# Optimization experiments

Measured on AMD Instinct MI355X. Metric: run time of the kernel, lower is better.

Reference implementation:

```python
import jax, jax.numpy as jnp
import numpy as np

H_G, W_G = 9, 25
N_NODES = H_G * W_G  # 225


def _grid_edge_index():
    # 8-connected grid graph INCLUDING self loops (di=dj=0), matching build_grid_edge_index.
    # PyG GATConv's remove_self_loops+add_self_loops leaves this edge set unchanged.
    edges = []
    for i in range(H_G):
        for j in range(W_G):
            nid = i * W_G + j
            for di in (-1, 0, 1):
                for dj in (-1, 0, 1):
                    ni, nj = i + di, j + dj
                    if 0 <= ni < H_G and 0 <= nj < W_G:
                        edges.append((nid, ni * W_G + nj))
    return jnp.asarray(np.array(edges, dtype=np.int32).T)  # [2, 1825]


def _gat(x, edge_index, W, a_src, a_dst, bias, concat):
    # x: [B, N, F_in]; W: [F_in, heads*d]; a_src/a_dst: [heads, d]
    B = x.shape[0]
    heads, d = a_src.shape
    h = (x @ W).reshape(B, N_NODES, heads, d)          # [B,N,H,D]
    src, dst = edge_index[0], edge_index[1]            # message flows src -> dst
    asrc = jnp.einsum('bnhd,hd->bnh', h, a_src)        # [B,N,H]
    adst = jnp.einsum('bnhd,hd->bnh', h, a_dst)
    e = jax.nn.leaky_relu(asrc[:, src] + adst[:, dst], 0.2)  # [B,E,H]
    et = jnp.transpose(e, (1, 0, 2))                   # [E,B,H] (segment ops over leading axis)
    m = jax.ops.segment_max(et, dst, num_segments=N_NODES)  # [N,B,H]
    ex = jnp.exp(et - m[dst])
    s = jax.ops.segment_sum(ex, dst, num_segments=N_NODES)
    alpha = ex / s[dst]                                # softmax over incoming edges per node
    ht = jnp.transpose(h, (1, 0, 2, 3))                # [N,B,H,D]
    out = jax.ops.segment_sum(alpha[..., None] * ht[src], dst, num_segments=N_NODES)  # [N,B,H,D]
    out = jnp.transpose(out, (1, 0, 2, 3))             # [B,N,H,D]
    if concat:
        out = out.reshape(B, N_NODES, heads * d)
    else:
        out = out.mean(axis=2)
    return out + bias


def setup_inputs() -> dict:
    key = jax.random.key(0)
    ks = jax.random.split(key, 16)
    B = 128
    s = 0.02
    inp = {
        'x4': jax.random.normal(ks[0], (B, 2048, 9, 25), dtype=jnp.float32),
        'pool_w': jax.random.normal(ks[1], (8, 2048), dtype=jnp.float32) * s,
        'pool_b': jnp.zeros((8,), dtype=jnp.float32),
        'gat1_w': jax.random.normal(ks[2], (8, 64), dtype=jnp.float32) * s,
        'gat1_asrc': jax.random.normal(ks[3], (4, 16), dtype=jnp.float32) * s,
        'gat1_adst': jax.random.normal(ks[4], (4, 16), dtype=jnp.float32) * s,
        'gat1_b': jnp.zeros((64,), dtype=jnp.float32),
        'gat2_w': jax.random.normal(ks[5], (64, 8), dtype=jnp.float32) * s,
        'gat2_asrc': jax.random.normal(ks[6], (1, 8), dtype=jnp.float32) * s,
        'gat2_adst': jax.random.normal(ks[7], (1, 8), dtype=jnp.float32) * s,
        'gat2_b': jnp.zeros((8,), dtype=jnp.float32),
        'w1': jax.random.normal(ks[8], (1800, 2048), dtype=jnp.float32) * 0.01,
        'b1': jnp.zeros((2048,), dtype=jnp.float32),
        'w2': jax.random.normal(ks[9], (2048, 20800), dtype=jnp.float32) * 0.01,
        'b2': jnp.zeros((20800,), dtype=jnp.float32),
        'edge_index': _grid_edge_index(),
    }
    return inp


def reference(x4, pool_w, pool_b, gat1_w, gat1_asrc, gat1_adst, gat1_b,
              gat2_w, gat2_asrc, gat2_adst, gat2_b, w1, b1, w2, b2, edge_index):
    B = x4.shape[0]
    # 1x1 conv pool: 2048 -> 8 channels (already 9x25, adaptive_avg_pool2d is identity)
    fea = jnp.einsum('bchw,oc->bohw', x4, pool_w) + pool_b[None, :, None, None]
    fea = fea.reshape(B, 8, N_NODES).transpose(0, 2, 1)  # [B, 225, 8]
    x1 = jax.nn.relu(_gat(fea, edge_index, gat1_w, gat1_asrc, gat1_adst, gat1_b, concat=True))
    x2 = _gat(x1, edge_index, gat2_w, gat2_asrc, gat2_adst, gat2_b, concat=False)  # [B,225,8]
    flat = x2.reshape(B, -1)                             # [B, 1800]
    hid = jax.nn.relu(flat @ w1 + b1)
    out = hid @ w2 + b2
    return out.reshape(-1, 100, 52, 4)
```

## Files before the change

kernel.cpp:

```cpp
#include <hip/hip_runtime.h>
#include <hip/hip_bf16.h>


typedef __attribute__((ext_vector_type(8))) short bh8_t;
typedef __attribute__((ext_vector_type(4))) float f32x4;

static __device__ __forceinline__ short f2bs(float f) {
    __hip_bfloat16 h = __float2bfloat16(f);
    return *reinterpret_cast<short*>(&h);
}
static __device__ __forceinline__ unsigned pack2(short a, short b) {
    return (unsigned)(unsigned short)a | ((unsigned)(unsigned short)b << 16);
}

__global__ __launch_bounds__(256) void pool_kernel(const float* __restrict__ x4,
                                                   const float* __restrict__ pool_w,
                                                   float* __restrict__ part) {
    const int b  = blockIdx.x >> 3;
    const int ch = blockIdx.x & 7;
    __shared__ __align__(16) float ws[256 * 8];
    const int tid = threadIdx.x;
    for (int i = tid; i < 2048; i += 256)
        ws[i] = pool_w[(i & 7) * 2048 + ch * 256 + (i >> 3)];
    __syncthreads();
    if (tid < 225) {
        const float* xp = x4 + ((size_t)b * 2048 + (size_t)ch * 256) * 225 + tid;
        float a0 = 0, a1 = 0, a2 = 0, a3 = 0, a4 = 0, a5 = 0, a6 = 0, a7 = 0;
#pragma unroll 8
        for (int c = 0; c < 256; ++c) {
            float v = xp[c * 225];
            const float4 wa = *reinterpret_cast<const float4*>(&ws[c * 8]);
            const float4 wb = *reinterpret_cast<const float4*>(&ws[c * 8 + 4]);
            a0 += v * wa.x; a1 += v * wa.y; a2 += v * wa.z; a3 += v * wa.w;
            a4 += v * wb.x; a5 += v * wb.y; a6 += v * wb.z; a7 += v * wb.w;
        }
        float* dst = part + (size_t)b * 14400 + ch * 1800 + tid * 8;
        dst[0] = a0; dst[1] = a1; dst[2] = a2; dst[3] = a3;
        dst[4] = a4; dst[5] = a5; dst[6] = a6; dst[7] = a7;
    }
}

__global__ __launch_bounds__(256) void gat1_kernel(const float* __restrict__ part,
                                                   const float* __restrict__ pool_b,
                                                   const float* __restrict__ w,
                                                   const float* __restrict__ a_src,
                                                   const float* __restrict__ a_dst,
                                                   const float* __restrict__ bias,
                                                   float* __restrict__ x1) {
    __shared__ __align__(16) float fea[1800];
    __shared__ __align__(16) float h[14400];
    const int b = blockIdx.x;
    const int tid = threadIdx.x;

    for (int i = tid; i < 1800; i += 256) {
        const float* p = part + (size_t)b * 14400 + i;
        float s = 0;
#pragma unroll
        for (int c = 0; c < 8; ++c) s += p[c * 1800];
        fea[i] = s + pool_b[i & 7];
    }
    __syncthreads();

    {
        const int o = tid & 63, mr = tid >> 6;
        float wv[8];
#pragma unroll
        for (int k = 0; k < 8; ++k) wv[k] = w[k * 64 + o];
        for (int n = mr; n < 225; n += 4) {
            float acc = 0;
#pragma unroll
            for (int k = 0; k < 8; ++k) acc += fea[n * 8 + k] * wv[k];
            h[n * 64 + o] = acc;
        }
    }
    __syncthreads();

    for (int t = tid; t < 900; t += 256) {
        const int n = t >> 2, hd = t & 3;
        const float* hp = &h[n * 64 + hd * 16];
        float as = 0, ad = 0;
#pragma unroll
        for (int d = 0; d < 16; ++d) {
            float hv = hp[d];
            as += hv * a_src[hd * 16 + d];
            ad += hv * a_dst[hd * 16 + d];
        }
        fea[t] = as;
        fea[900 + t] = ad;
    }
    __syncthreads();

    for (int task = tid; task < 900; task += 256) {
        const int n = task >> 2, hd = task & 3;
        const int i = n / 25, j = n % 25;
        const float adn = fea[900 + task];
        float e[9];
        int sid[9];
        float mx = -1e30f;
#pragma unroll
        for (int t9 = 0; t9 < 9; ++t9) {
            const int di = t9 / 3 - 1, dj = t9 % 3 - 1;
            const int ni = i + di, nj = j + dj;
            const bool valid = ((unsigned)ni < 9u) && ((unsigned)nj < 25u);
            const int s = valid ? ni * 25 + nj : n;
            sid[t9] = s;
            float ev = fea[s * 4 + hd] + adn;
            ev = ev >= 0.f ? ev : 0.2f * ev;
            e[t9] = valid ? ev : -1e30f;
            mx = fmaxf(mx, e[t9]);
        }
        float sum = 0;
#pragma unroll
        for (int t9 = 0; t9 < 9; ++t9) {
            float ex = __expf(e[t9] - mx);
            e[t9] = ex;
            sum += ex;
        }
        const float inv = 1.f / sum;
        float out[16] = {};
#pragma unroll
        for (int t9 = 0; t9 < 9; ++t9) {
            const float al = e[t9] * inv;
            const float* hp = &h[sid[t9] * 64 + hd * 16];
#pragma unroll
            for (int d = 0; d < 16; ++d) out[d] += al * hp[d];
        }
        float* dst = x1 + (size_t)b * 14400 + n * 64 + hd * 16;
        const float* bp = bias + hd * 16;
#pragma unroll
        for (int d = 0; d < 16; ++d) dst[d] = fmaxf(out[d] + bp[d], 0.f);
    }
}

__global__ __launch_bounds__(256) void gat2_kernel(const float* __restrict__ x1,
                                                   const float* __restrict__ w,
                                                   const float* __restrict__ a_src,
                                                   const float* __restrict__ a_dst,
                                                   const float* __restrict__ bias,
                                                   short* __restrict__ flat) {
    __shared__ __align__(16) float xs[14400];
    __shared__ __align__(16) float h[1800];
    const int b = blockIdx.x;
    const int tid = threadIdx.x;
    for (int i = tid; i < 14400; i += 256) xs[i] = x1[(size_t)b * 14400 + i];
    __syncthreads();
    for (int t = tid; t < 1800; t += 256) {
        const int o = t & 7, n = t >> 3;
        float acc = 0;
#pragma unroll 8
        for (int k = 0; k < 64; ++k) acc += xs[n * 64 + k] * w[k * 8 + o];
        h[t] = acc;
    }
    __syncthreads();
    if (tid < 225) {
        const int n = tid, i = n / 25, j = n % 25;
        float av[8], dv[8];
#pragma unroll
        for (int d = 0; d < 8; ++d) { av[d] = a_src[d]; dv[d] = a_dst[d]; }
        float adn = 0;
#pragma unroll
        for (int d = 0; d < 8; ++d) adn += h[n * 8 + d] * dv[d];
        float e[9];
        int sid[9];
        float mx = -1e30f;
#pragma unroll
        for (int t9 = 0; t9 < 9; ++t9) {
            const int di = t9 / 3 - 1, dj = t9 % 3 - 1;
            const int ni = i + di, nj = j + dj;
            const bool valid = ((unsigned)ni < 9u) && ((unsigned)nj < 25u);
            const int s = valid ? ni * 25 + nj : n;
            sid[t9] = s;
            float as = 0;
#pragma unroll
            for (int d = 0; d < 8; ++d) as += h[s * 8 + d] * av[d];
            float ev = as + adn;
            ev = ev >= 0.f ? ev : 0.2f * ev;
            e[t9] = valid ? ev : -1e30f;
            mx = fmaxf(mx, e[t9]);
        }
        float sum = 0;
#pragma unroll
        for (int t9 = 0; t9 < 9; ++t9) {
            float ex = __expf(e[t9] - mx);
            e[t9] = ex;
            sum += ex;
        }
        const float inv = 1.f / sum;
        float out[8] = {};
#pragma unroll
        for (int t9 = 0; t9 < 9; ++t9) {
            const float al = e[t9] * inv;
            const float* hp = &h[sid[t9] * 8];
#pragma unroll
            for (int d = 0; d < 8; ++d) out[d] += al * hp[d];
        }
        short* dst = flat + (size_t)b * 1800 + n * 8;
#pragma unroll
        for (int d = 0; d < 8; ++d) dst[d] = f2bs(out[d] + bias[d]);
    }
}

template <int BN, int MT, int NT, int NWN, bool RELU, bool OUT_BF16>
__global__ __launch_bounds__(256) void gemm_mfma(const short* __restrict__ A,
                                                 const float* __restrict__ Wf,
                                                 const float* __restrict__ bias,
                                                 void* __restrict__ outp,
                                                 int K, int N) {
    constexpr int LDT = 40;
    __shared__ __align__(16) short sA[128 * LDT];
    __shared__ __align__(16) short sB[BN * LDT];
    const int tid = threadIdx.x;
    const int lane = tid & 63;
    const int wave = tid >> 6;
    const int n0 = blockIdx.x * BN;
    const int wm0 = (wave / NWN) * (MT * 16);
    const int wn0 = (wave % NWN) * (NT * 16);
    const int lm = lane & 15;
    const int lkb = (lane >> 4) * 8;

    const int am = tid >> 1;
    const int akh = tid & 1;
    constexpr int EPT = (32 * BN) / 256;
    const int bn_ = tid % BN;
    const int bk0 = (tid / BN) * EPT;

    f32x4 acc[MT][NT] = {};

    const int nkt = (K + 31) >> 5;
    for (int kt = 0; kt < nkt; ++kt) {
        const int k0 = kt << 5;
        if (k0 + 32 <= K) {
            const uint4* src = reinterpret_cast<const uint4*>(A + (size_t)am * K + k0 + akh * 16);
            uint4 v0 = src[0];
            uint4 v1 = src[1];
            float bv[EPT];
#pragma unroll
            for (int jj = 0; jj < EPT; ++jj)
                bv[jj] = Wf[(size_t)(k0 + bk0 + jj) * N + n0 + bn_];
            uint4* dstA = reinterpret_cast<uint4*>(&sA[am * LDT + akh * 16]);
            dstA[0] = v0;
            dstA[1] = v1;
            unsigned uw[EPT / 2];
#pragma unroll
            for (int jj = 0; jj < EPT / 2; ++jj)
                uw[jj] = pack2(f2bs(bv[2 * jj]), f2bs(bv[2 * jj + 1]));
            if constexpr (EPT == 8) {
                uint4 u;
                u.x = uw[0]; u.y = uw[1]; u.z = uw[2]; u.w = uw[3];
                *reinterpret_cast<uint4*>(&sB[bn_ * LDT + bk0]) = u;
            } else {
                *reinterpret_cast<unsigned*>(&sB[bn_ * LDT + bk0]) = uw[0];
            }
        } else {
#pragma unroll
            for (int jj = 0; jj < 16; ++jj) {
                const int kk = k0 + akh * 16 + jj;
                sA[am * LDT + akh * 16 + jj] = (kk < K) ? A[(size_t)am * K + kk] : (short)0;
            }
#pragma unroll
            for (int jj = 0; jj < EPT; ++jj) {
                const int kk = k0 + bk0 + jj;
                const float v = (kk < K) ? Wf[(size_t)kk * N + n0 + bn_] : 0.f;
                sB[bn_ * LDT + bk0 + jj] = f2bs(v);
            }
        }
        __syncthreads();
        bh8_t bfr[NT];
#pragma unroll
        for (int nt = 0; nt < NT; ++nt)
            bfr[nt] = *reinterpret_cast<const bh8_t*>(&sB[(wn0 + nt * 16 + lm) * LDT + lkb]);
#pragma unroll
        for (int mt = 0; mt < MT; ++mt) {
            bh8_t afr = *reinterpret_cast<const bh8_t*>(&sA[(wm0 + mt * 16 + lm) * LDT + lkb]);
#pragma unroll
            for (int nt = 0; nt < NT; ++nt)
                acc[mt][nt] = __builtin_amdgcn_mfma_f32_16x16x32_bf16(afr, bfr[nt], acc[mt][nt], 0, 0, 0);
        }
        __syncthreads();
    }
    const int rg = lane >> 4;
#pragma unroll
    for (int nt = 0; nt < NT; ++nt) {
        const int n = n0 + wn0 + nt * 16 + lm;
        const float bv = bias[n];
#pragma unroll
        for (int mt = 0; mt < MT; ++mt) {
#pragma unroll
            for (int r = 0; r < 4; ++r) {
                const int m = wm0 + mt * 16 + rg * 4 + r;
                float v = acc[mt][nt][r] + bv;
                if (RELU) v = fmaxf(v, 0.f);
                if (OUT_BF16)
                    reinterpret_cast<short*>(outp)[(size_t)m * N + n] = f2bs(v);
                else
                    reinterpret_cast<float*>(outp)[(size_t)m * N + n] = v;
            }
        }
    }
}

extern "C" void kernel_launch(void* const* d_in, const int* in_sizes, int n_in,
                              void* d_out, int out_size, void* d_ws, size_t ws_size,
                              hipStream_t stream) {
    const float* x4        = (const float*)d_in[0];
    const float* pool_w    = (const float*)d_in[1];
    const float* pool_b    = (const float*)d_in[2];
    const float* gat1_w    = (const float*)d_in[3];
    const float* gat1_asrc = (const float*)d_in[4];
    const float* gat1_adst = (const float*)d_in[5];
    const float* gat1_b    = (const float*)d_in[6];
    const float* gat2_w    = (const float*)d_in[7];
    const float* gat2_asrc = (const float*)d_in[8];
    const float* gat2_adst = (const float*)d_in[9];
    const float* gat2_b    = (const float*)d_in[10];
    const float* w1        = (const float*)d_in[11];
    const float* b1        = (const float*)d_in[12];
    const float* w2        = (const float*)d_in[13];
    const float* b2        = (const float*)d_in[14];
    float* out = (float*)d_out;

    char* ws = (char*)d_ws;
    float* part = (float*)ws;
    float* x1   = (float*)(ws + 7372800);
    short* flat = (short*)(ws + 14745600);
    short* hid  = (short*)(ws + 15206400);

    pool_kernel<<<1024, 256, 0, stream>>>(x4, pool_w, part);
    gat1_kernel<<<128, 256, 0, stream>>>(part, pool_b, gat1_w, gat1_asrc, gat1_adst, gat1_b, x1);
    gat2_kernel<<<128, 256, 0, stream>>>(x1, gat2_w, gat2_asrc, gat2_adst, gat2_b, flat);
    gemm_mfma<16, 2, 1, 1, true, true><<<128, 256, 0, stream>>>(flat, w1, b1, (void*)hid, 1800, 2048);
    gemm_mfma<64, 4, 2, 2, false, false><<<325, 256, 0, stream>>>(hid, w2, b2, (void*)out, 2048, 20800);
}
```

Measured before the change: 568.6 us.

## Prefetch GEMM tiles into registers, swizzle GAT LDS, vectorize stores, retile w2 GEMM

```diff
diff --git a/kernel.cpp b/kernel.cpp
--- a/kernel.cpp
+++ b/kernel.cpp
@@ -11,6 +11,12 @@
 }
 static __device__ __forceinline__ unsigned pack2(short a, short b) {
     return (unsigned)(unsigned short)a | ((unsigned)(unsigned short)b << 16);
+}
+static __device__ __forceinline__ int swz64(int n, int o) {
+    return n * 64 + ((((o >> 2) ^ (n & 15)) << 2) | (o & 3));
+}
+static __device__ __forceinline__ int swzg(int n, int g) {
+    return n * 64 + ((g ^ (n & 15)) << 2);
 }
 
 __global__ __launch_bounds__(256) void pool_kernel(const float* __restrict__ x4,
@@ -18,26 +24,29 @@
                                                    float* __restrict__ part) {
     const int b  = blockIdx.x >> 3;
     const int ch = blockIdx.x & 7;
-    __shared__ __align__(16) float ws[256 * 8];
     const int tid = threadIdx.x;
-    for (int i = tid; i < 2048; i += 256)
-        ws[i] = pool_w[(i & 7) * 2048 + ch * 256 + (i >> 3)];
-    __syncthreads();
-    if (tid < 225) {
-        const float* xp = x4 + ((size_t)b * 2048 + (size_t)ch * 256) * 225 + tid;
-        float a0 = 0, a1 = 0, a2 = 0, a3 = 0, a4 = 0, a5 = 0, a6 = 0, a7 = 0;
+    if (tid >= 225) return;
+    const float* xp = x4 + ((size_t)b * 2048 + (size_t)ch * 256) * 225 + tid;
+    const float* w0 = pool_w + 0 * 2048 + ch * 256;
+    const float* w1 = pool_w + 1 * 2048 + ch * 256;
+    const float* w2 = pool_w + 2 * 2048 + ch * 256;
+    const float* w3 = pool_w + 3 * 2048 + ch * 256;
+    const float* w4 = pool_w + 4 * 2048 + ch * 256;
+    const float* w5 = pool_w + 5 * 2048 + ch * 256;
+    const float* w6 = pool_w + 6 * 2048 + ch * 256;
+    const float* w7 = pool_w + 7 * 2048 + ch * 256;
+    float a0 = 0, a1 = 0, a2 = 0, a3 = 0, a4 = 0, a5 = 0, a6 = 0, a7 = 0;
 #pragma unroll 8
-        for (int c = 0; c < 256; ++c) {
-            float v = xp[c * 225];
-            const float4 wa = *reinterpret_cast<const float4*>(&ws[c * 8]);
-            const float4 wb = *reinterpret_cast<const float4*>(&ws[c * 8 + 4]);
-            a0 += v * wa.x; a1 += v * wa.y; a2 += v * wa.z; a3 += v * wa.w;
-            a4 += v * wb.x; a5 += v * wb.y; a6 += v * wb.z; a7 += v * wb.w;
-        }
-        float* dst = part + (size_t)b * 14400 + ch * 1800 + tid * 8;
-        dst[0] = a0; dst[1] = a1; dst[2] = a2; dst[3] = a3;
-        dst[4] = a4; dst[5] = a5; dst[6] = a6; dst[7] = a7;
-    }
+    for (int c = 0; c < 256; ++c) {
+        const float v = xp[c * 225];
+        a0 += v * w0[c]; a1 += v * w1[c]; a2 += v * w2[c]; a3 += v * w3[c];
+        a4 += v * w4[c]; a5 += v * w5[c]; a6 += v * w6[c]; a7 += v * w7[c];
+    }
+    float* dst = part + (size_t)b * 14400 + ch * 1800 + tid * 8;
+    float4 r0; r0.x = a0; r0.y = a1; r0.z = a2; r0.w = a3;
+    float4 r1; r1.x = a4; r1.y = a5; r1.z = a6; r1.w = a7;
+    *reinterpret_cast<float4*>(dst) = r0;
+    *reinterpret_cast<float4*>(dst + 4) = r1;
 }
 
 __global__ __launch_bounds__(256) void gat1_kernel(const float* __restrict__ part,
@@ -70,65 +79,90 @@
             float acc = 0;
 #pragma unroll
             for (int k = 0; k < 8; ++k) acc += fea[n * 8 + k] * wv[k];
-            h[n * 64 + o] = acc;
-        }
-    }
-    __syncthreads();
-
-    for (int t = tid; t < 900; t += 256) {
-        const int n = t >> 2, hd = t & 3;
-        const float* hp = &h[n * 64 + hd * 16];
-        float as = 0, ad = 0;
-#pragma unroll
-        for (int d = 0; d < 16; ++d) {
-            float hv = hp[d];
-            as += hv * a_src[hd * 16 + d];
-            ad += hv * a_dst[hd * 16 + d];
-        }
-        fea[t] = as;
-        fea[900 + t] = ad;
-    }
-    __syncthreads();
-
-    for (int task = tid; task < 900; task += 256) {
-        const int n = task >> 2, hd = task & 3;
-        const int i = n / 25, j = n % 25;
-        const float adn = fea[900 + task];
-        float e[9];
-        int sid[9];
-        float mx = -1e30f;
-#pragma unroll
-        for (int t9 = 0; t9 < 9; ++t9) {
-            const int di = t9 / 3 - 1, dj = t9 % 3 - 1;
-            const int ni = i + di, nj = j + dj;
-            const bool valid = ((unsigned)ni < 9u) && ((unsigned)nj < 25u);
-            const int s = valid ? ni * 25 + nj : n;
-            sid[t9] = s;
-            float ev = fea[s * 4 + hd] + adn;
-            ev = ev >= 0.f ? ev : 0.2f * ev;
-            e[t9] = valid ? ev : -1e30f;
-            mx = fmaxf(mx, e[t9]);
-        }
-        float sum = 0;
-#pragma unroll
-        for (int t9 = 0; t9 < 9; ++t9) {
-            float ex = __expf(e[t9] - mx);
-            e[t9] = ex;
-            sum += ex;
-        }
-        const float inv = 1.f / sum;
-        float out[16] = {};
-#pragma unroll
-        for (int t9 = 0; t9 < 9; ++t9) {
-            const float al = e[t9] * inv;
-            const float* hp = &h[sid[t9] * 64 + hd * 16];
-#pragma unroll
-            for (int d = 0; d < 16; ++d) out[d] += al * hp[d];
-        }
-        float* dst = x1 + (size_t)b * 14400 + n * 64 + hd * 16;
-        const float* bp = bias + hd * 16;
-#pragma unroll
-        for (int d = 0; d < 16; ++d) dst[d] = fmaxf(out[d] + bp[d], 0.f);
+            h[swz64(n, o)] = acc;
+        }
+    }
+    __syncthreads();
+
+    {
+        const int hd = tid & 3;
+        float4 asw[4], adw[4];
+#pragma unroll
+        for (int j = 0; j < 4; ++j) {
+            asw[j] = *reinterpret_cast<const float4*>(a_src + hd * 16 + 4 * j);
+            adw[j] = *reinterpret_cast<const float4*>(a_dst + hd * 16 + 4 * j);
+        }
+        for (int t = tid; t < 900; t += 256) {
+            const int n = t >> 2;
+            float as = 0, ad = 0;
+#pragma unroll
+            for (int j = 0; j < 4; ++j) {
+                const float4 hv = *reinterpret_cast<const float4*>(&h[swzg(n, 4 * hd + j)]);
+                as += hv.x * asw[j].x + hv.y * asw[j].y + hv.z * asw[j].z + hv.w * asw[j].w;
+                ad += hv.x * adw[j].x + hv.y * adw[j].y + hv.z * adw[j].z + hv.w * adw[j].w;
+            }
+            fea[t] = as;
+            fea[900 + t] = ad;
+        }
+    }
+    __syncthreads();
+
+    {
+        const int hd = tid & 3;
+        float4 b4[4];
+#pragma unroll
+        for (int j = 0; j < 4; ++j)
+            b4[j] = *reinterpret_cast<const float4*>(bias + hd * 16 + 4 * j);
+        for (int task = tid; task < 900; task += 256) {
+            const int n = task >> 2;
+            const int i = n / 25, j25 = n % 25;
+            const float adn = fea[900 + task];
+            float e[9];
+            int sid[9];
+            float mx = -1e30f;
+#pragma unroll
+            for (int t9 = 0; t9 < 9; ++t9) {
+                const int di = t9 / 3 - 1, dj = t9 % 3 - 1;
+                const int ni = i + di, nj = j25 + dj;
+                const bool valid = ((unsigned)ni < 9u) && ((unsigned)nj < 25u);
+                const int s = valid ? ni * 25 + nj : n;
+                sid[t9] = s;
+                float ev = fea[s * 4 + hd] + adn;
+                ev = ev >= 0.f ? ev : 0.2f * ev;
+                e[t9] = valid ? ev : -1e30f;
+                mx = fmaxf(mx, e[t9]);
+            }
+            float sum = 0;
+#pragma unroll
+            for (int t9 = 0; t9 < 9; ++t9) {
+                float ex = __expf(e[t9] - mx);
+                e[t9] = ex;
+                sum += ex;
+            }
+            const float inv = 1.f / sum;
+            float4 o4[4] = {};
+#pragma unroll
+            for (int t9 = 0; t9 < 9; ++t9) {
+                const float al = e[t9] * inv;
+                const int s = sid[t9];
+#pragma unroll
+                for (int jj = 0; jj < 4; ++jj) {
+                    const float4 hv = *reinterpret_cast<const float4*>(&h[swzg(s, 4 * hd + jj)]);
+                    o4[jj].x += al * hv.x; o4[jj].y += al * hv.y;
+                    o4[jj].z += al * hv.z; o4[jj].w += al * hv.w;
+                }
+            }
+            float* dst = x1 + (size_t)b * 14400 + n * 64 + hd * 16;
+#pragma unroll
+            for (int jj = 0; jj < 4; ++jj) {
+                float4 r;
+                r.x = fmaxf(o4[jj].x + b4[jj].x, 0.f);
+                r.y = fmaxf(o4[jj].y + b4[jj].y, 0.f);
+                r.z = fmaxf(o4[jj].z + b4[jj].z, 0.f);
+                r.w = fmaxf(o4[jj].w + b4[jj].w, 0.f);
+                *reinterpret_cast<float4*>(dst + 4 * jj) = r;
+            }
+        }
     }
 }
 
@@ -139,17 +173,26 @@
                                                    const float* __restrict__ bias,
                                                    short* __restrict__ flat) {
     __shared__ __align__(16) float xs[14400];
-    __shared__ __align__(16) float h[1800];
+    __shared__ __align__(16) float h2[8 * 232];
     const int b = blockIdx.x;
     const int tid = threadIdx.x;
-    for (int i = tid; i < 14400; i += 256) xs[i] = x1[(size_t)b * 14400 + i];
+    for (int i4 = tid; i4 < 3600; i4 += 256) {
+        const int n = i4 >> 4, g0 = i4 & 15;
+        const float4 v = *reinterpret_cast<const float4*>(&x1[(size_t)b * 14400 + (i4 << 2)]);
+        *reinterpret_cast<float4*>(&xs[swzg(n, g0)]) = v;
+    }
     __syncthreads();
     for (int t = tid; t < 1800; t += 256) {
         const int o = t & 7, n = t >> 3;
         float acc = 0;
-#pragma unroll 8
-        for (int k = 0; k < 64; ++k) acc += xs[n * 64 + k] * w[k * 8 + o];
-        h[t] = acc;
+#pragma unroll
+        for (int jj = 0; jj < 16; ++jj) {
+            const float4 xv = *reinterpret_cast<const float4*>(&xs[swzg(n, jj)]);
+            const int k = 4 * jj;
+            acc += xv.x * w[k * 8 + o] + xv.y * w[(k + 1) * 8 + o]
+                 + xv.z * w[(k + 2) * 8 + o] + xv.w * w[(k + 3) * 8 + o];
+        }
+        h2[o * 232 + n] = acc;
     }
     __syncthreads();
     if (tid < 225) {
@@ -159,7 +202,7 @@
         for (int d = 0; d < 8; ++d) { av[d] = a_src[d]; dv[d] = a_dst[d]; }
         float adn = 0;
 #pragma unroll
-        for (int d = 0; d < 8; ++d) adn += h[n * 8 + d] * dv[d];
+        for (int d = 0; d < 8; ++d) adn += h2[d * 232 + n] * dv[d];
         float e[9];
         int sid[9];
         float mx = -1e30f;
@@ -172,7 +215,7 @@
             sid[t9] = s;
             float as = 0;
 #pragma unroll
-            for (int d = 0; d < 8; ++d) as += h[s * 8 + d] * av[d];
+            for (int d = 0; d < 8; ++d) as += h2[d * 232 + s] * av[d];
             float ev = as + adn;
             ev = ev >= 0.f ? ev : 0.2f * ev;
             e[t9] = valid ? ev : -1e30f;
@@ -190,13 +233,15 @@
 #pragma unroll
         for (int t9 = 0; t9 < 9; ++t9) {
             const float al = e[t9] * inv;
-            const float* hp = &h[sid[t9] * 8];
-#pragma unroll
-            for (int d = 0; d < 8; ++d) out[d] += al * hp[d];
-        }
-        short* dst = flat + (size_t)b * 1800 + n * 8;
-#pragma unroll
-        for (int d = 0; d < 8; ++d) dst[d] = f2bs(out[d] + bias[d]);
+#pragma unroll
+            for (int d = 0; d < 8; ++d) out[d] += al * h2[d * 232 + sid[t9]];
+        }
+        unsigned u[4];
+#pragma unroll
+        for (int p = 0; p < 4; ++p)
+            u[p] = pack2(f2bs(out[2 * p] + bias[2 * p]), f2bs(out[2 * p + 1] + bias[2 * p + 1]));
+        uint4 uv; uv.x = u[0]; uv.y = u[1]; uv.z = u[2]; uv.w = u[3];
+        *reinterpret_cast<uint4*>(flat + (size_t)b * 1800 + n * 8) = uv;
     }
 }
 
@@ -207,6 +252,7 @@
                                                  void* __restrict__ outp,
                                                  int K, int N) {
     constexpr int LDT = 40;
+    constexpr int EPT = (32 * BN) / 256;
     __shared__ __align__(16) short sA[128 * LDT];
     __shared__ __align__(16) short sB[BN * LDT];
     const int tid = threadIdx.x;
@@ -220,51 +266,62 @@
 
     const int am = tid >> 1;
     const int akh = tid & 1;
-    constexpr int EPT = (32 * BN) / 256;
     const int bn_ = tid % BN;
     const int bk0 = (tid / BN) * EPT;
 
-    f32x4 acc[MT][NT] = {};
-
+    union { uint4 v[2]; short s[16]; } pa;
+    float pb[EPT];
     const int nkt = (K + 31) >> 5;
-    for (int kt = 0; kt < nkt; ++kt) {
+
+    auto loadg = [&](int kt) {
         const int k0 = kt << 5;
         if (k0 + 32 <= K) {
             const uint4* src = reinterpret_cast<const uint4*>(A + (size_t)am * K + k0 + akh * 16);
-            uint4 v0 = src[0];
-            uint4 v1 = src[1];
-            float bv[EPT];
+            pa.v[0] = src[0];
+            pa.v[1] = src[1];
 #pragma unroll
             for (int jj = 0; jj < EPT; ++jj)
-                bv[jj] = Wf[(size_t)(k0 + bk0 + jj) * N + n0 + bn_];
-            uint4* dstA = reinterpret_cast<uint4*>(&sA[am * LDT + akh * 16]);
-            dstA[0] = v0;
-            dstA[1] = v1;
-            unsigned uw[EPT / 2];
-#pragma unroll
-            for (int jj = 0; jj < EPT / 2; ++jj)
-                uw[jj] = pack2(f2bs(bv[2 * jj]), f2bs(bv[2 * jj + 1]));
-            if constexpr (EPT == 8) {
-                uint4 u;
-                u.x = uw[0]; u.y = uw[1]; u.z = uw[2]; u.w = uw[3];
-                *reinterpret_cast<uint4*>(&sB[bn_ * LDT + bk0]) = u;
-            } else {
-                *reinterpret_cast<unsigned*>(&sB[bn_ * LDT + bk0]) = uw[0];
-            }
+                pb[jj] = Wf[(size_t)(k0 + bk0 + jj) * N + n0 + bn_];
         } else {
 #pragma unroll
             for (int jj = 0; jj < 16; ++jj) {
                 const int kk = k0 + akh * 16 + jj;
-                sA[am * LDT + akh * 16 + jj] = (kk < K) ? A[(size_t)am * K + kk] : (short)0;
+                pa.s[jj] = (kk < K) ? A[(size_t)am * K + kk] : (short)0;
             }
 #pragma unroll
             for (int jj = 0; jj < EPT; ++jj) {
                 const int kk = k0 + bk0 + jj;
-                const float v = (kk < K) ? Wf[(size_t)kk * N + n0 + bn_] : 0.f;
-                sB[bn_ * LDT + bk0 + jj] = f2bs(v);
-            }
-        }
+                pb[jj] = (kk < K) ? Wf[(size_t)kk * N + n0 + bn_] : 0.f;
+            }
+        }
+    };
+
+    f32x4 acc[MT][NT] = {};
+    loadg(0);
+
+    for (int kt = 0; kt < nkt; ++kt) {
         __syncthreads();
+        {
+            uint4* dstA = reinterpret_cast<uint4*>(&sA[am * LDT + akh * 16]);
+            dstA[0] = pa.v[0];
+            dstA[1] = pa.v[1];
+            unsigned uw[EPT / 2];
+#pragma unroll
+            for (int jj = 0; jj < EPT / 2; ++jj)
+                uw[jj] = pack2(f2bs(pb[2 * jj]), f2bs(pb[2 * jj + 1]));
+            short* bdst = &sB[bn_ * LDT + bk0];
+            if constexpr (EPT == 8) {
+                uint4 u; u.x = uw[0]; u.y = uw[1]; u.z = uw[2]; u.w = uw[3];
+                *reinterpret_cast<uint4*>(bdst) = u;
+            } else if constexpr (EPT == 4) {
+                uint2 u; u.x = uw[0]; u.y = uw[1];
+                *reinterpret_cast<uint2*>(bdst) = u;
+            } else {
+                *reinterpret_cast<unsigned*>(bdst) = uw[0];
+            }
+        }
+        __syncthreads();
+        if (kt + 1 < nkt) loadg(kt + 1);
         bh8_t bfr[NT];
 #pragma unroll
         for (int nt = 0; nt < NT; ++nt)
@@ -276,7 +333,6 @@
             for (int nt = 0; nt < NT; ++nt)
                 acc[mt][nt] = __builtin_amdgcn_mfma_f32_16x16x32_bf16(afr, bfr[nt], acc[mt][nt], 0, 0, 0);
         }
-        __syncthreads();
     }
     const int rg = lane >> 4;
 #pragma unroll
@@ -329,5 +385,5 @@
     gat1_kernel<<<128, 256, 0, stream>>>(part, pool_b, gat1_w, gat1_asrc, gat1_adst, gat1_b, x1);
     gat2_kernel<<<128, 256, 0, stream>>>(x1, gat2_w, gat2_asrc, gat2_adst, gat2_b, flat);
     gemm_mfma<16, 2, 1, 1, true, true><<<128, 256, 0, stream>>>(flat, w1, b1, (void*)hid, 1800, 2048);
-    gemm_mfma<64, 4, 2, 2, false, false><<<325, 256, 0, stream>>>(hid, w2, b2, (void*)out, 2048, 20800);
-}
+    gemm_mfma<32, 4, 1, 2, false, false><<<650, 256, 0, stream>>>(hid, w2, b2, (void*)out, 2048, 20800);
+}
```

Result: no change. 577.7 us (+1.6%).
